# Optimization experiments

Hardware: AMD Instinct MI355X
Metric: run time of the kernel (lower is better)

Reference implementation:

```python
import jax, jax.numpy as jnp
import numpy as np

DIM = 1024
HEADS = 16
HEAD_DIM = DIM // HEADS


def setup_inputs() -> dict:
    key = jax.random.key(0)
    k1, k2, k3 = jax.random.split(key, 3)
    x = jax.random.normal(k1, (4, 4096, DIM), dtype=jnp.float32)
    # nn.Linear weights; stored as [out, in] in torch, apply as x @ W.T
    w_qkv = jax.random.normal(k2, (3 * DIM, DIM), dtype=jnp.float32) * (1.0 / np.sqrt(DIM))
    w_out = jax.random.normal(k3, (DIM, DIM), dtype=jnp.float32) * (1.0 / np.sqrt(DIM))
    return {"x": x, "w_qkv": w_qkv, "w_out": w_out}


def _feature_map(t):
    # ELU + 1 (always positive)
    return jax.nn.elu(t) + 1.0


def reference(x, w_qkv, w_out):
    b, n, _ = x.shape
    qkv = x @ w_qkv.T  # [b, n, 3*dim]
    q, k, v = jnp.split(qkv, 3, axis=-1)
    # [b, n, dim] -> [b, h, n, d]
    def to_heads(t):
        return t.reshape(b, n, HEADS, HEAD_DIM).transpose(0, 2, 1, 3)
    q, k, v = to_heads(q), to_heads(k), to_heads(v)
    q = _feature_map(q)
    k = _feature_map(k)
    # KV state: [b, h, d, e]
    kv = jnp.einsum('bhnd,bhne->bhde', k, v)
    out = jnp.einsum('bhnd,bhde->bhne', q, kv)  # [b, h, n, e]
    k_sum = k.sum(axis=2)  # [b, h, d]
    normalizer = jnp.einsum('bhnd,bhd->bhn', q, k_sum)  # [b, h, n]
    out = out / (normalizer[..., None] + 1e-06)
    out = out.transpose(0, 2, 1, 3).reshape(b, n, DIM)
    return out @ w_out.T
```

## Files before the change

### kernel.cpp

```cpp
#include <hip/hip_runtime.h>
#include <hip/hip_bf16.h>
#include <stdint.h>

typedef __attribute__((ext_vector_type(8))) short short8;
typedef __attribute__((ext_vector_type(4))) float f32x4;
typedef __attribute__((ext_vector_type(4))) unsigned short ushort4_t;

#define SEG 16

__device__ __forceinline__ float bf2f(unsigned short u) {
  unsigned int x = ((unsigned int)u) << 16;
  return __uint_as_float(x);
}
__device__ __forceinline__ unsigned short f2bf(float f) {
  unsigned int u = __float_as_uint(f);
  u += 0x7fffu + ((u >> 16) & 1u);
  return (unsigned short)(u >> 16);
}

__device__ __forceinline__ void gload16(const unsigned short* g, unsigned short* l) {
  __builtin_amdgcn_global_load_lds(
      (const __attribute__((address_space(1))) void*)g,
      (__attribute__((address_space(3))) void*)l, 16, 0, 0);
}

__global__ void cast_f32_bf16(const float* __restrict__ in,
                              unsigned short* __restrict__ out, int n4) {
  const int stride = gridDim.x * blockDim.x;
  for (int i = blockIdx.x * blockDim.x + threadIdx.x; i < n4; i += stride) {
    const float4 v = ((const float4*)in)[i];
    ushort4_t o;
    o[0] = f2bf(v.x); o[1] = f2bf(v.y); o[2] = f2bf(v.z); o[3] = f2bf(v.w);
    ((ushort4_t*)out)[i] = o;
  }
}

#define MIDBAR() do { __builtin_amdgcn_sched_barrier(0); __builtin_amdgcn_s_barrier(); } while (0)
#define ENDBAR() do { __builtin_amdgcn_s_barrier(); __builtin_amdgcn_sched_barrier(0); } while (0)
#define ENDBARV() do { asm volatile("s_waitcnt vmcnt(4)" ::: "memory"); \
                       __builtin_amdgcn_s_barrier(); __builtin_amdgcn_sched_barrier(0); } while (0)

template <typename OutT>
__global__ __launch_bounds__(512, 2) void gemm8p(
    const unsigned short* __restrict__ A, const unsigned short* __restrict__ Bm,
    OutT* __restrict__ C, int M, int N, int K, int ldc, int fm_cols) {
  __shared__ unsigned short lds[65536];
  unsigned short* A0 = lds;
  unsigned short* B0 = lds + 16384;
  unsigned short* A1 = lds + 32768;
  unsigned short* B1 = lds + 49152;
  const int tid = threadIdx.x;
  const int lane = tid & 63;
  const int w = tid >> 6;
  const int wr = w >> 2, wc = w & 3;
  const int gx = gridDim.x;
  const int nwg = gx * gridDim.y;
  const int hwid = blockIdx.y * gx + blockIdx.x;
  const int cpx = nwg >> 3;
  const int L = (hwid & 7) * cpx + (hwid >> 3);
  const int bx = L % gx, by = L / gx;
  const size_t arow0 = (size_t)by * 256;
  const size_t bcol0 = (size_t)bx * 256;
  const int nt = K >> 6;
  const int nit = nt >> 1;

  const int sc8 = ((lane & 7) ^ (lane >> 3)) << 3;
  const unsigned short* Abase = A + (arow0 + (lane >> 3)) * K + sc8;
  const unsigned short* Bbase = Bm + (bcol0 + (lane >> 3)) * K + sc8;

  auto stage = [&](int kt, const unsigned short* mb, unsigned short* region, int half) {
    const int ktw = (kt >= nt) ? kt - nt : kt;
    const int rb = half * 128 + w * 16;
    const unsigned short* s = mb + (size_t)rb * K + ktw * 64;
    gload16(s, region + rb * 64);
    gload16(s + (size_t)8 * K, region + (rb + 8) * 64);
  };

  short8 af[4][2];
  short8 bfv[4][2];
  f32x4 acc[8][4] = {};
  const int fr = lane & 15;
  const int kc = lane >> 4;

  auto readA = [&](const unsigned short* bufA, int mh) {
#pragma unroll
    for (int mm = 0; mm < 4; ++mm) {
      const int r = wr * 128 + (mh * 4 + mm) * 16 + fr;
#pragma unroll
      for (int ks = 0; ks < 2; ++ks)
        af[mm][ks] = *(const short8*)&bufA[r * 64 + (((ks * 4 + kc) ^ (fr & 7)) << 3)];
    }
  };
  auto readB = [&](const unsigned short* bufB, int nh) {
#pragma unroll
    for (int nn = 0; nn < 2; ++nn) {
      const int n = nh * 2 + nn;
      const int r = wc * 64 + n * 16 + fr;
#pragma unroll
      for (int ks = 0; ks < 2; ++ks)
        bfv[n][ks] = *(const short8*)&bufB[16384 * 0 + r * 64 + (((ks * 4 + kc) ^ (fr & 7)) << 3)];
    }
  };
  auto quad = [&](int mh, int nh) {
    __builtin_amdgcn_s_setprio(1);
#pragma unroll
    for (int mm = 0; mm < 4; ++mm)
#pragma unroll
      for (int nn = 0; nn < 2; ++nn) {
        f32x4& a = acc[mh * 4 + mm][nh * 2 + nn];
        a = __builtin_amdgcn_mfma_f32_16x16x32_bf16(af[mm][0], bfv[nh * 2 + nn][0], a, 0, 0, 0);
        a = __builtin_amdgcn_mfma_f32_16x16x32_bf16(af[mm][1], bfv[nh * 2 + nn][1], a, 0, 0, 0);
      }
    __builtin_amdgcn_s_setprio(0);
  };

  stage(0, Abase, A0, 0); stage(0, Abase, A0, 1);
  stage(0, Bbase, B0, 0); stage(0, Bbase, B0, 1);
  stage(1, Bbase, B1, 0); stage(1, Bbase, B1, 1);
  asm volatile("s_waitcnt vmcnt(0)" ::: "memory");
  __builtin_amdgcn_s_barrier();
  __builtin_amdgcn_sched_barrier(0);

  for (int i2 = 0; i2 < nit; ++i2) {
    const int t0 = i2 * 2;
    readA(A0, 0); readB(B0, 0);
    stage(t0 + 1, Abase, A1, 0);
    MIDBAR(); quad(0, 0); ENDBAR();

    readB(B0, 1);
    stage(t0 + 1, Abase, A1, 1);
    MIDBAR(); quad(0, 1); ENDBAR();

    readA(A0, 1);
    stage(t0 + 2, Bbase, B0, 0);
    MIDBAR(); quad(1, 0); ENDBAR();

    stage(t0 + 2, Bbase, B0, 1);
    MIDBAR(); quad(1, 1); ENDBARV();
    readA(A1, 0); readB(B1, 0);
    stage(t0 + 2, Abase, A0, 0);
    MIDBAR(); quad(0, 0); ENDBAR();

    readB(B1, 1);
    stage(t0 + 2, Abase, A0, 1);
    MIDBAR(); quad(0, 1); ENDBAR();

    readA(A1, 1);
    stage(t0 + 3, Bbase, B1, 0);
    MIDBAR(); quad(1, 0); ENDBAR();

    stage(t0 + 3, Bbase, B1, 1);
    MIDBAR(); quad(1, 1); ENDBARV();
  }

  const int qq = lane >> 4;
#pragma unroll
  for (int m = 0; m < 8; ++m) {
#pragma unroll
    for (int n = 0; n < 4; ++n) {
      const int col = (int)bcol0 + wc * 64 + n * 16 + fr;
      const bool dofm = col < fm_cols;
#pragma unroll
      for (int j = 0; j < 4; ++j) {
        const int row = (int)arow0 + wr * 128 + m * 16 + qq * 4 + j;
        float x = acc[m][n][j];
        if (dofm) x = (x > 0.f) ? x + 1.f : __expf(x);
        if constexpr (sizeof(OutT) == 2) {
          C[(size_t)row * ldc + col] = (OutT)f2bf(x);
        } else {
          C[(size_t)row * ldc + col] = x;
        }
      }
    }
  }
}

__global__ __launch_bounds__(256) void kv_partial(
    const unsigned short* __restrict__ kvmat, float* __restrict__ kvp,
    float* __restrict__ ksp) {
  const int blk = blockIdx.x;
  const int bh = blk >> 4;
  const int seg = blk & (SEG - 1);
  const int b = bh >> 4, h = bh & 15;
  const int rows = 4096 / SEG;
  const size_t row0 = (size_t)b * 4096 + (size_t)seg * rows;
  const unsigned short* kb = kvmat + row0 * 2048 + h * 64;
  const unsigned short* vb = kvmat + row0 * 2048 + 1024 + h * 64;
  __shared__ float kl[32][64];
  __shared__ float vl[32][64];
  const int tid = threadIdx.x;
  const int d0 = (tid >> 4) * 4, e0 = (tid & 15) * 4;
  const int lr = tid >> 3, lc = (tid & 7) * 8;
  float accm[4][4] = {};
  float ksacc[4] = {0.f, 0.f, 0.f, 0.f};

  for (int c = 0; c < rows; c += 32) {
    __syncthreads();
    {
      const short8 k8 = *(const short8*)(kb + (size_t)(c + lr) * 2048 + lc);
      const short8 v8 = *(const short8*)(vb + (size_t)(c + lr) * 2048 + lc);
#pragma unroll
      for (int j = 0; j < 8; ++j) {
        kl[lr][lc + j] = bf2f((unsigned short)k8[j]);
        vl[lr][lc + j] = bf2f((unsigned short)v8[j]);
      }
    }
    __syncthreads();
#pragma unroll
    for (int r = 0; r < 32; ++r) {
      const f32x4 kd = *(const f32x4*)&kl[r][d0];
      const f32x4 ve = *(const f32x4*)&vl[r][e0];
#pragma unroll
      for (int i = 0; i < 4; ++i) {
        ksacc[i] += kd[i];
#pragma unroll
        for (int j = 0; j < 4; ++j) accm[i][j] += kd[i] * ve[j];
      }
    }
  }
  float* kvout = kvp + ((size_t)seg * 64 + bh) * 4096;
#pragma unroll
  for (int i = 0; i < 4; ++i) {
    f32x4 o = {accm[i][0], accm[i][1], accm[i][2], accm[i][3]};
    *(f32x4*)&kvout[(d0 + i) * 64 + e0] = o;
  }
  if ((tid & 15) == 0) {
#pragma unroll
    for (int i = 0; i < 4; ++i)
      ksp[((size_t)seg * 64 + bh) * 64 + d0 + i] = ksacc[i];
  }
}

__global__ void kv_reduce_bf(const float* __restrict__ kvp, const float* __restrict__ ksp,
                             unsigned short* __restrict__ kvb) {
  const int idx = blockIdx.x * 256 + threadIdx.x;
  if (idx >= 64 * 80 * 64) return;
  const int bh = idx / 5120, r = idx % 5120, e = r >> 6, d = r & 63;
  float s = 0.f;
  if (e < 64) {
    for (int g = 0; g < SEG; ++g) s += kvp[((size_t)g * 64 + bh) * 4096 + d * 64 + e];
  } else if (e == 64) {
    for (int g = 0; g < SEG; ++g) s += ksp[((size_t)g * 64 + bh) * 64 + d];
  }
  kvb[idx] = f2bf(s);
}

__global__ __launch_bounds__(256) void attn_mfma(
    const unsigned short* __restrict__ q,
    const unsigned short* __restrict__ kvb,
    unsigned short* __restrict__ att) {
  const int bh = blockIdx.x >> 4;
  const int rt = blockIdx.x & 15;
  const int b = bh >> 4, h = bh & 15;
  __shared__ unsigned short As[2 * 256 * 32];
  __shared__ unsigned short Bs[2 * 80 * 32];
  const int tid = threadIdx.x, lane = tid & 63, wave = tid >> 6;
  const int l4 = lane >> 2;
  const int c8 = (lane & 3) * 8;
  const size_t qrow0 = (size_t)b * 4096 + (size_t)rt * 256;
  const unsigned short* Ab = q + (qrow0 + wave * 64 + l4) * 1024 + h * 64 + c8;
  unsigned short* AsW = As;
#pragma unroll
  for (int ks = 0; ks < 2; ++ks)
#pragma unroll
    for (int i = 0; i < 4; ++i)
      gload16(Ab + (size_t)i * 16 * 1024 + ks * 32,
              AsW + ks * 8192 + wave * 2048 + i * 512);
  for (int c = tid; c < 640; c += 256) {
    const int m0 = c * 8, ks = m0 / 2560, rr = m0 % 2560, e = rr / 32, dk = rr % 32;
    *(short8*)&Bs[m0] = *(const short8*)&kvb[(size_t)bh * 5120 + e * 64 + ks * 32 + dk];
  }
  __syncthreads();

  const int fr = lane & 15, ko = (lane >> 4) * 8;
  short8 af[4][2], bfv[5][2];
#pragma unroll
  for (int m = 0; m < 4; ++m)
#pragma unroll
    for (int ks = 0; ks < 2; ++ks)
      af[m][ks] = *(const short8*)&As[ks * 8192 + (wave * 64 + m * 16 + fr) * 32 + ko];
#pragma unroll
  for (int n = 0; n < 5; ++n)
#pragma unroll
    for (int ks = 0; ks < 2; ++ks)
      bfv[n][ks] = *(const short8*)&Bs[ks * 2560 + (n * 16 + fr) * 32 + ko];
  f32x4 acc[4][5] = {};
#pragma unroll
  for (int m = 0; m < 4; ++m)
#pragma unroll
    for (int n = 0; n < 5; ++n) {
      acc[m][n] = __builtin_amdgcn_mfma_f32_16x16x32_bf16(af[m][0], bfv[n][0], acc[m][n], 0, 0, 0);
      acc[m][n] = __builtin_amdgcn_mfma_f32_16x16x32_bf16(af[m][1], bfv[n][1], acc[m][n], 0, 0, 0);
    }

  const int qq = lane >> 4;
#pragma unroll
  for (int m = 0; m < 4; ++m) {
    f32x4 rnv;
#pragma unroll
    for (int j = 0; j < 4; ++j) {
      const float nv = __shfl(acc[m][4][j], lane & 48);
      rnv[j] = 1.f / (nv + 1e-6f);
    }
    const size_t row = qrow0 + wave * 64 + m * 16 + qq * 4;
#pragma unroll
    for (int n = 0; n < 4; ++n)
#pragma unroll
      for (int j = 0; j < 4; ++j)
        att[(row + j) * 1024 + h * 64 + n * 16 + fr] = f2bf(acc[m][n][j] * rnv[j]);
  }
}

extern "C" void kernel_launch(void* const* d_in, const int* in_sizes, int n_in,
                              void* d_out, int out_size, void* d_ws, size_t ws_size,
                              hipStream_t stream) {
  const float* x = (const float*)d_in[0];
  const float* wqkv = (const float*)d_in[1];
  const float* wout = (const float*)d_in[2];
  float* out = (float*)d_out;

  char* ws = (char*)d_ws;
  size_t off = 0;
  auto alloc = [&](size_t bytes) -> void* {
    void* p = ws + off;
    off += (bytes + 255) & ~(size_t)255;
    return p;
  };
  unsigned short* xbf    = (unsigned short*)alloc((size_t)16384 * 1024 * 2);
  unsigned short* wqkvbf = (unsigned short*)alloc((size_t)3072 * 1024 * 2);
  unsigned short* woutbf = (unsigned short*)alloc((size_t)1024 * 1024 * 2);
  unsigned short* big    = (unsigned short*)alloc((size_t)16384 * 2048 * 2);
  float* kvp = (float*)alloc((size_t)SEG * 64 * 4096 * 4);
  float* ksp = (float*)alloc((size_t)SEG * 64 * 64 * 4);
  unsigned short* kvb = (unsigned short*)alloc((size_t)64 * 80 * 64 * 2);
  unsigned short* qbuf = big;
  unsigned short* att  = big + (size_t)16384 * 1024;

  cast_f32_bf16<<<2048, 256, 0, stream>>>(x, xbf, 16384 * 1024 / 4);
  cast_f32_bf16<<<1024, 256, 0, stream>>>(wqkv, wqkvbf, 3072 * 1024 / 4);
  cast_f32_bf16<<<512, 256, 0, stream>>>(wout, woutbf, 1024 * 1024 / 4);

  gemm8p<unsigned short><<<dim3(2048 / 256, 16384 / 256), 512, 0, stream>>>(
      xbf, wqkvbf + (size_t)1024 * 1024, big, 16384, 2048, 1024, 2048, 1024);

  kv_partial<<<64 * SEG, 256, 0, stream>>>(big, kvp, ksp);
  kv_reduce_bf<<<1280, 256, 0, stream>>>(kvp, ksp, kvb);

  gemm8p<unsigned short><<<dim3(1024 / 256, 16384 / 256), 512, 0, stream>>>(
      xbf, wqkvbf, qbuf, 16384, 1024, 1024, 1024, 1024);

  attn_mfma<<<64 * 16, 256, 0, stream>>>(qbuf, kvb, att);

  gemm8p<float><<<dim3(1024 / 256, 16384 / 256), 512, 0, stream>>>(
      att, woutbf, out, 16384, 1024, 1024, 1024, 0);
}
```

Baseline: 258.1 us.

## Add 256x128 triple-buffered GEMM for K/V projection with higher occupancy

Adds a new GEMM kernel that uses 256x128 output tiles, a K-step of 32 and a three-stage LDS ring buffer, targeting four workgroups per CU. It replaces the 256x256 eight-phase GEMM only for the K/V projection. Smaller tiles double the grid size and give more occupancy to hide latency. The cost is lower data reuse per tile and one barrier per K step. The edits to the old GEMM are only cosmetic renames.

```diff
diff --git a/kernel.cpp b/kernel.cpp
--- a/kernel.cpp
+++ b/kernel.cpp
@@ -23,6 +23,11 @@
       (const __attribute__((address_space(1))) void*)g,
       (__attribute__((address_space(3))) void*)l, 16, 0, 0);
 }
+
+#define MIDBAR() do { __builtin_amdgcn_sched_barrier(0); __builtin_amdgcn_s_barrier(); } while (0)
+#define ENDBAR() do { __builtin_amdgcn_s_barrier(); __builtin_amdgcn_sched_barrier(0); } while (0)
+#define ENDBARV4() do { asm volatile("s_waitcnt vmcnt(4)" ::: "memory"); \
+                        __builtin_amdgcn_s_barrier(); __builtin_amdgcn_sched_barrier(0); } while (0)
 
 __global__ void cast_f32_bf16(const float* __restrict__ in,
                               unsigned short* __restrict__ out, int n4) {
@@ -35,10 +40,107 @@
   }
 }
 
-#define MIDBAR() do { __builtin_amdgcn_sched_barrier(0); __builtin_amdgcn_s_barrier(); } while (0)
-#define ENDBAR() do { __builtin_amdgcn_s_barrier(); __builtin_amdgcn_sched_barrier(0); } while (0)
-#define ENDBARV() do { asm volatile("s_waitcnt vmcnt(4)" ::: "memory"); \
-                       __builtin_amdgcn_s_barrier(); __builtin_amdgcn_sched_barrier(0); } while (0)
+template <typename OutT>
+__global__ __launch_bounds__(512, 4) void gemm_v4(
+    const unsigned short* __restrict__ A, const unsigned short* __restrict__ Bm,
+    OutT* __restrict__ C, int M, int N, int K, int ldc, int fm_cols) {
+  __shared__ unsigned short lds[3 * 12288];
+  const int tid = threadIdx.x;
+  const int lane = tid & 63;
+  const int w = tid >> 6;
+  const int wr = w >> 1, wc = w & 1;
+  const int gx = gridDim.x;
+  const int nwg = gx * gridDim.y;
+  const int hwid = blockIdx.y * gx + blockIdx.x;
+  const int cpx = nwg >> 3;
+  const int L = (hwid & 7) * cpx + (hwid >> 3);
+  const int bx = L % gx, by = L / gx;
+  const size_t arow0 = (size_t)by * 256;
+  const size_t bcol0 = (size_t)bx * 128;
+  const int nt = K >> 5;
+
+  const int rl = lane >> 2;
+  const int sce = (((lane & 3) ^ (rl & 3) ^ ((rl >> 2) & 1)) << 3);
+  const unsigned short* Ab0 = A + (arow0 + w * 16 + rl) * K + sce;
+  const unsigned short* Ab1 = A + (arow0 + 128 + w * 16 + rl) * K + sce;
+  const unsigned short* Bb0 = Bm + (bcol0 + w * 16 + rl) * K + sce;
+
+  auto stage = [&](int kt, unsigned short* buf) {
+    const int k0 = (kt < nt ? kt : kt - nt) << 5;
+    gload16(Ab0 + k0, buf + w * 512);
+    gload16(Ab1 + k0, buf + 4096 + w * 512);
+    gload16(Bb0 + k0, buf + 8192 + w * 512);
+  };
+
+  f32x4 acc[4][4] = {};
+  const int fr = lane & 15;
+  const int kc = lane >> 4;
+
+  auto rdA = [&](const unsigned short* buf, int mm) {
+    const int r = wr * 64 + mm * 16 + fr;
+    return *(const short8*)&buf[r * 32 + ((kc ^ (fr & 3) ^ ((fr >> 2) & 1)) << 3)];
+  };
+  auto rdB = [&](const unsigned short* buf, int nn) {
+    const int r = wc * 64 + nn * 16 + fr;
+    return *(const short8*)&buf[8192 + r * 32 + ((kc ^ (fr & 3) ^ ((fr >> 2) & 1)) << 3)];
+  };
+
+  stage(0, lds);
+  stage(1, lds + 12288);
+  asm volatile("s_waitcnt vmcnt(3)" ::: "memory");
+  __builtin_amdgcn_s_barrier();
+  __builtin_amdgcn_sched_barrier(0);
+
+  for (int t = 0; t < nt; ++t) {
+    const unsigned short* cur = lds + (t % 3) * 12288;
+    unsigned short* nxt = lds + ((t + 2) % 3) * 12288;
+    stage(t + 2, nxt);
+    const short8 af0 = rdA(cur, 0), af1 = rdA(cur, 1), af2 = rdA(cur, 2), af3 = rdA(cur, 3);
+    const short8 bf0 = rdB(cur, 0), bf1 = rdB(cur, 1), bf2 = rdB(cur, 2), bf3 = rdB(cur, 3);
+    __builtin_amdgcn_s_setprio(1);
+    acc[0][0] = __builtin_amdgcn_mfma_f32_16x16x32_bf16(af0, bf0, acc[0][0], 0, 0, 0);
+    acc[0][1] = __builtin_amdgcn_mfma_f32_16x16x32_bf16(af0, bf1, acc[0][1], 0, 0, 0);
+    acc[1][0] = __builtin_amdgcn_mfma_f32_16x16x32_bf16(af1, bf0, acc[1][0], 0, 0, 0);
+    acc[1][1] = __builtin_amdgcn_mfma_f32_16x16x32_bf16(af1, bf1, acc[1][1], 0, 0, 0);
+    acc[0][2] = __builtin_amdgcn_mfma_f32_16x16x32_bf16(af0, bf2, acc[0][2], 0, 0, 0);
+    acc[0][3] = __builtin_amdgcn_mfma_f32_16x16x32_bf16(af0, bf3, acc[0][3], 0, 0, 0);
+    acc[1][2] = __builtin_amdgcn_mfma_f32_16x16x32_bf16(af1, bf2, acc[1][2], 0, 0, 0);
+    acc[1][3] = __builtin_amdgcn_mfma_f32_16x16x32_bf16(af1, bf3, acc[1][3], 0, 0, 0);
+    acc[2][0] = __builtin_amdgcn_mfma_f32_16x16x32_bf16(af2, bf0, acc[2][0], 0, 0, 0);
+    acc[2][1] = __builtin_amdgcn_mfma_f32_16x16x32_bf16(af2, bf1, acc[2][1], 0, 0, 0);
+    acc[3][0] = __builtin_amdgcn_mfma_f32_16x16x32_bf16(af3, bf0, acc[3][0], 0, 0, 0);
+    acc[3][1] = __builtin_amdgcn_mfma_f32_16x16x32_bf16(af3, bf1, acc[3][1], 0, 0, 0);
+    acc[2][2] = __builtin_amdgcn_mfma_f32_16x16x32_bf16(af2, bf2, acc[2][2], 0, 0, 0);
+    acc[2][3] = __builtin_amdgcn_mfma_f32_16x16x32_bf16(af2, bf3, acc[2][3], 0, 0, 0);
+    acc[3][2] = __builtin_amdgcn_mfma_f32_16x16x32_bf16(af3, bf2, acc[3][2], 0, 0, 0);
+    acc[3][3] = __builtin_amdgcn_mfma_f32_16x16x32_bf16(af3, bf3, acc[3][3], 0, 0, 0);
+    __builtin_amdgcn_s_setprio(0);
+    asm volatile("s_waitcnt vmcnt(3)" ::: "memory");
+    __builtin_amdgcn_s_barrier();
+    __builtin_amdgcn_sched_barrier(0);
+  }
+
+  const int qq = lane >> 4;
+#pragma unroll
+  for (int m = 0; m < 4; ++m) {
+#pragma unroll
+    for (int n = 0; n < 4; ++n) {
+      const int col = (int)bcol0 + wc * 64 + n * 16 + fr;
+      const bool dofm = col < fm_cols;
+#pragma unroll
+      for (int j = 0; j < 4; ++j) {
+        const int row = (int)arow0 + wr * 64 + m * 16 + qq * 4 + j;
+        float x = acc[m][n][j];
+        if (dofm) x = (x > 0.f) ? x + 1.f : __expf(x);
+        if constexpr (sizeof(OutT) == 2) {
+          C[(size_t)row * ldc + col] = (OutT)f2bf(x);
+        } else {
+          C[(size_t)row * ldc + col] = x;
+        }
+      }
+    }
+  }
+}
 
 template <typename OutT>
 __global__ __launch_bounds__(512, 2) void gemm8p(
@@ -98,7 +200,7 @@
       const int r = wc * 64 + n * 16 + fr;
 #pragma unroll
       for (int ks = 0; ks < 2; ++ks)
-        bfv[n][ks] = *(const short8*)&bufB[16384 * 0 + r * 64 + (((ks * 4 + kc) ^ (fr & 7)) << 3)];
+        bfv[n][ks] = *(const short8*)&bufB[r * 64 + (((ks * 4 + kc) ^ (fr & 7)) << 3)];
     }
   };
   auto quad = [&](int mh, int nh) {
@@ -136,7 +238,8 @@
     MIDBAR(); quad(1, 0); ENDBAR();
 
     stage(t0 + 2, Bbase, B0, 1);
-    MIDBAR(); quad(1, 1); ENDBARV();
+    MIDBAR(); quad(1, 1); ENDBARV4();
+
     readA(A1, 0); readB(B1, 0);
     stage(t0 + 2, Abase, A0, 0);
     MIDBAR(); quad(0, 0); ENDBAR();
@@ -150,7 +253,7 @@
     MIDBAR(); quad(1, 0); ENDBAR();
 
     stage(t0 + 3, Bbase, B1, 1);
-    MIDBAR(); quad(1, 1); ENDBARV();
+    MIDBAR(); quad(1, 1); ENDBARV4();
   }
 
   const int qq = lane >> 4;
@@ -340,7 +443,7 @@
   cast_f32_bf16<<<1024, 256, 0, stream>>>(wqkv, wqkvbf, 3072 * 1024 / 4);
   cast_f32_bf16<<<512, 256, 0, stream>>>(wout, woutbf, 1024 * 1024 / 4);
 
-  gemm8p<unsigned short><<<dim3(2048 / 256, 16384 / 256), 512, 0, stream>>>(
+  gemm_v4<unsigned short><<<dim3(2048 / 128, 16384 / 256), 512, 0, stream>>>(
       xbf, wqkvbf + (size_t)1024 * 1024, big, 16384, 2048, 1024, 2048, 1024);
 
   kv_partial<<<64 * SEG, 256, 0, stream>>>(big, kvp, ksp);
```

Result: slower. 264.2 us (+2.4%).
